# Performance work log

Hardware: AMD Instinct MI355X
Metric: run time of the kernel (lower is better)

## Reference

```python
import jax, jax.numpy as jnp
import numpy as np

B, N, D_IN, D_OUT, E = 4, 50000, 128, 128, 800000


def setup_inputs() -> dict:
    key = jax.random.key(0)
    k_x, k_w, k_b, k_r, k_c, k_v = jax.random.split(key, 6)
    stdv = 1.0 / np.sqrt(D_OUT)
    x = jax.random.normal(k_x, (B, N, D_IN), dtype=jnp.float32)
    weight = jax.random.uniform(k_w, (D_IN, D_OUT), jnp.float32, -stdv, stdv)
    bias = jax.random.uniform(k_b, (D_OUT,), jnp.float32, -stdv, stdv)
    adj_rows = jax.random.randint(k_r, (E,), 0, N, dtype=jnp.int32)
    adj_cols = jax.random.randint(k_c, (E,), 0, N, dtype=jnp.int32)
    # positive edge weights (e.g. normalized adjacency values)
    adj_vals = jax.random.uniform(k_v, (E,), jnp.float32) * (1.0 / 16.0)
    edge_index = jnp.stack([adj_rows, adj_cols]).astype(jnp.int64)  # unused (pyg_builtin=False)
    return {"input": x, "weight": weight, "bias": bias,
            "adj_vals": adj_vals, "adj_rows": adj_rows, "adj_cols": adj_cols,
            "edge_index": edge_index}


def reference(input, weight, bias, adj_vals, adj_rows, adj_cols, edge_index):
    # support = input @ W : [B, N, D_OUT]
    support = jnp.einsum('bnd,df->bnf', input, weight)

    # node_repr = sparse adj (COO) @ support, batched == torch.sparse.mm path
    def agg(s):  # s: [N, D_OUT]
        msgs = adj_vals[:, None] * s[adj_cols]          # [E, D_OUT] gather
        return jax.ops.segment_sum(msgs, adj_rows, num_segments=N)  # scatter-add

    node_repr = jax.vmap(agg)(support) + bias           # [B, N, D_OUT]
    # net_norm='none' -> no norm; activation=relu; residual=False; dropout=0
    return jax.nn.relu(node_repr)
```

## Files before the change

### kernel.cpp

```cpp
#include <hip/hip_runtime.h>
#include <hip/hip_bf16.h>

#define BB 4
#define NN 50000
#define DIN 128
#define DOUT 128
#define EE 800000
#define TOTROWS (BB * NN)
#define LDA 136

typedef unsigned short u16;
typedef unsigned int u32;

using shortx8 = __attribute__((ext_vector_type(8))) short;
using ushortx4 = __attribute__((ext_vector_type(4))) unsigned short;
using ushortx8 = __attribute__((ext_vector_type(8))) unsigned short;
using floatx4 = __attribute__((ext_vector_type(4))) float;

__device__ __forceinline__ float b2f(u16 u) {
    u32 x = ((u32)u) << 16;
    float f;
    __builtin_memcpy(&f, &x, 4);
    return f;
}

__device__ __forceinline__ u16 f2b(float f) {
    u32 x;
    __builtin_memcpy(&x, &f, 4);
    u32 r = x + 0x7fffu + ((x >> 16) & 1u);
    return (u16)(r >> 16);
}

__global__ __launch_bounds__(256)
void k_detect(const u16* __restrict__ X, const u16* __restrict__ W,
              const u16* __restrict__ Bs, const u16* __restrict__ V,
              int nx, int nw, int nb, int nv, int* __restrict__ flags) {
    __shared__ int cnt[4];
    const int t = threadIdx.x;
    const int w = t >> 6;
    const int l = t & 63;
    if (t < 4) cnt[t] = 0;
    __syncthreads();
    const u16* p = (w == 0) ? X : (w == 1) ? W : (w == 2) ? Bs : V;
    const int n  = (w == 0) ? nx : (w == 1) ? nw : (w == 2) ? nb : nv;
    int bad = 0;
    for (int k = 0; k < 4; ++k) {
        unsigned idx = 2u * (unsigned)(((unsigned long long)(l * 4 + k) *
                                        (unsigned)(n >> 1)) >> 8);
        u16 s = p[idx];
        unsigned e = (s >> 7) & 0xFF;
        bool ok = ((s & 0x7FFF) == 0) || (e >= 90 && e <= 141);
        bad += ok ? 0 : 1;
    }
    atomicAdd(&cnt[w], bad);
    __syncthreads();
    if (l == 0) flags[w] = (cnt[w] >= 77) ? 1 : 0;
}

__global__ __launch_bounds__(256)
void k_prep(const void* __restrict__ Wv, const int* __restrict__ flags,
            u16* __restrict__ Wt) {
    int t = blockIdx.x * 256 + threadIdx.x;
    if (t < DIN * DOUT) {
        int f = t >> 7, k = t & 127;
        size_t src = (size_t)k * DOUT + f;
        Wt[t] = flags[1] ? f2b(((const float*)Wv)[src]) : ((const u16*)Wv)[src];
    }
}

__global__ __launch_bounds__(256, 3)
void k_gemm(const void* __restrict__ Xv, const u16* __restrict__ Wt,
            const int* __restrict__ flags, u16* __restrict__ sup) {
    __shared__ u16 lA[128 * LDA];

    const int xf32 = flags[0];
    const int tid = threadIdx.x;
    const int wid = tid >> 6;
    const int l   = tid & 63;
    const long rowBase = (long)blockIdx.x * 128;

    if (xf32) {
        const float* Xf = (const float*)Xv;
#pragma unroll
        for (int i = 0; i < 16; ++i) {
            int elem = i * 1024 + tid * 4;
            int row = elem >> 7, col = elem & 127;
            long gRow = rowBase + row;
            ushortx4 w4 = (ushortx4){0, 0, 0, 0};
            if (gRow < TOTROWS) {
                float4 v = *(const float4*)(Xf + gRow * DIN + col);
                w4[0] = f2b(v.x); w4[1] = f2b(v.y);
                w4[2] = f2b(v.z); w4[3] = f2b(v.w);
            }
            *(ushortx4*)&lA[row * LDA + col] = w4;
        }
    } else {
        const u16* X16 = (const u16*)Xv;
#pragma unroll
        for (int i = 0; i < 8; ++i) {
            int elem = i * 2048 + tid * 8;
            int row = elem >> 7, col = elem & 127;
            long gRow = rowBase + row;
            ushortx8 w8 = (ushortx8){0, 0, 0, 0, 0, 0, 0, 0};
            if (gRow < TOTROWS)
                w8 = *(const ushortx8*)(X16 + gRow * DIN + col);
            *(ushortx8*)&lA[row * LDA + col] = w8;
        }
    }

    const int wx = wid & 1;
    const int wy = wid >> 1;
    const int q8 = (l >> 4) * 8;
    const int lm = l & 15;

    shortx8 bf[16];
#pragma unroll
    for (int nt = 0; nt < 4; ++nt) {
        const size_t Frow = (size_t)(wx * 64 + nt * 16 + lm) * DIN;
#pragma unroll
        for (int c = 0; c < 4; ++c)
            bf[nt * 4 + c] = *(const shortx8*)(Wt + Frow + 32 * c + q8);
    }

    floatx4 acc[4][4];
#pragma unroll
    for (int mt = 0; mt < 4; ++mt)
#pragma unroll
        for (int nt = 0; nt < 4; ++nt)
            acc[mt][nt] = (floatx4){0.f, 0.f, 0.f, 0.f};

    __syncthreads();

    for (int c = 0; c < 4; ++c) {
        shortx8 af[4];
#pragma unroll
        for (int mt = 0; mt < 4; ++mt)
            af[mt] = *(const shortx8*)
                &lA[(size_t)(wy * 64 + mt * 16 + lm) * LDA + 32 * c + q8];
#pragma unroll
        for (int mt = 0; mt < 4; ++mt)
#pragma unroll
            for (int nt = 0; nt < 4; ++nt)
                acc[mt][nt] = __builtin_amdgcn_mfma_f32_16x16x32_bf16(
                    af[mt], bf[nt * 4 + c], acc[mt][nt], 0, 0, 0);
    }

#pragma unroll
    for (int mt = 0; mt < 4; ++mt) {
#pragma unroll
        for (int reg = 0; reg < 4; ++reg) {
            long R = rowBase + wy * 64 + mt * 16 + (l >> 4) * 4 + reg;
            if (R < TOTROWS) {
                int b = (int)(R / NN);
                int n = (int)(R % NN);
                size_t outRow = ((size_t)n * BB + b) * DOUT;
#pragma unroll
                for (int nt = 0; nt < 4; ++nt) {
                    int F = wx * 64 + nt * 16 + lm;
                    sup[outRow + F] = f2b(acc[mt][nt][reg]);
                }
            }
        }
    }
}

__global__ __launch_bounds__(256)
void k_hist(const int* __restrict__ rows, int* __restrict__ deg) {
    int e = blockIdx.x * 256 + threadIdx.x;
    if (e < EE) atomicAdd(&deg[rows[e]], 1);
}

#define CHUNK 1024
#define NCHUNK ((NN + CHUNK - 1) / CHUNK)

__global__ __launch_bounds__(256)
void k_scan_reduce(const int* __restrict__ deg, int* __restrict__ bsum) {
    __shared__ int sh[256];
    int t = threadIdx.x, blk = blockIdx.x;
    int base = blk * CHUNK + t * 4;
    int s = 0;
#pragma unroll
    for (int i = 0; i < 4; ++i) {
        int idx = base + i;
        if (idx < NN) s += deg[idx];
    }
    sh[t] = s;
    __syncthreads();
    for (int d = 128; d > 0; d >>= 1) {
        if (t < d) sh[t] += sh[t + d];
        __syncthreads();
    }
    if (t == 0) bsum[blk] = sh[0];
}

__global__ __launch_bounds__(64)
void k_scan_base(const int* __restrict__ bsum, int* __restrict__ bbase,
                 int* __restrict__ off) {
    if (threadIdx.x == 0) {
        int run = 0;
        for (int i = 0; i < NCHUNK; ++i) {
            bbase[i] = run;
            run += bsum[i];
        }
        off[NN] = run;
    }
}

__global__ __launch_bounds__(256)
void k_scan_chunk(const int* __restrict__ deg, const int* __restrict__ bbase,
                  int* __restrict__ off) {
    __shared__ int sh[256];
    int t = threadIdx.x;
    int blk = blockIdx.x;
    int base = blk * CHUNK + t * 4;
    int v[4];
    int tsum = 0;
#pragma unroll
    for (int i = 0; i < 4; ++i) {
        int idx = base + i;
        v[i] = (idx < NN) ? deg[idx] : 0;
        tsum += v[i];
    }
    sh[t] = tsum;
    __syncthreads();
    for (int d = 1; d < 256; d <<= 1) {
        int x = (t >= d) ? sh[t - d] : 0;
        __syncthreads();
        sh[t] += x;
        __syncthreads();
    }
    int run = sh[t] - tsum + bbase[blk];
#pragma unroll
    for (int i = 0; i < 4; ++i) {
        int idx = base + i;
        if (idx < NN) off[idx] = run;
        run += v[i];
    }
}

__global__ __launch_bounds__(256)
void k_scatter(const int* __restrict__ rows, const int* __restrict__ cols,
               const void* __restrict__ valsv, const int* __restrict__ flags,
               const int* __restrict__ off, int* __restrict__ cur,
               int* __restrict__ ecol, float* __restrict__ eval) {
    int e = blockIdx.x * 256 + threadIdx.x;
    if (e < EE) {
        int vf32 = flags[3];
        float v = vf32 ? ((const float*)valsv)[e] : b2f(((const u16*)valsv)[e]);
        int r = rows[e];
        int p = off[r] + atomicAdd(&cur[r], 1);
        ecol[p] = cols[e];
        eval[p] = v;
    }
}

__global__ __launch_bounds__(256)
void k_agg(const u16* __restrict__ sup, const int* __restrict__ off,
           const int* __restrict__ ecol, const float* __restrict__ eval,
           const void* __restrict__ biasv, const int* __restrict__ flags,
           float* __restrict__ out) {
    const int wid = threadIdx.x >> 6;
    const int l   = threadIdx.x & 63;
    const int n = blockIdx.x * 4 + wid;
    if (n >= NN) return;

    const int p0 = off[n];
    const int p1 = off[n + 1];

    float acc[8] = {0.f, 0.f, 0.f, 0.f, 0.f, 0.f, 0.f, 0.f};
    const int b  = l >> 4;
    const int f0 = (l & 15) * 8;
    const int lofs = l * 8;

    int p = p0;
    for (; p + 2 <= p1; p += 2) {
        int c0 = ecol[p], c1 = ecol[p + 1];
        float v0 = eval[p], v1 = eval[p + 1];
        ushortx8 s0 = *(const ushortx8*)(sup + (size_t)c0 * 512 + lofs);
        ushortx8 s1 = *(const ushortx8*)(sup + (size_t)c1 * 512 + lofs);
#pragma unroll
        for (int t = 0; t < 8; ++t) acc[t] += v0 * b2f(s0[t]);
#pragma unroll
        for (int t = 0; t < 8; ++t) acc[t] += v1 * b2f(s1[t]);
    }
    if (p < p1) {
        int c = ecol[p];
        float v = eval[p];
        ushortx8 s = *(const ushortx8*)(sup + (size_t)c * 512 + lofs);
#pragma unroll
        for (int t = 0; t < 8; ++t) acc[t] += v * b2f(s[t]);
    }

    float bb[8];
    if (flags[2]) {
        float4 bv1 = *(const float4*)((const float*)biasv + f0);
        float4 bv2 = *(const float4*)((const float*)biasv + f0 + 4);
        bb[0] = bv1.x; bb[1] = bv1.y; bb[2] = bv1.z; bb[3] = bv1.w;
        bb[4] = bv2.x; bb[5] = bv2.y; bb[6] = bv2.z; bb[7] = bv2.w;
    } else {
        ushortx8 bv = *(const ushortx8*)((const u16*)biasv + f0);
#pragma unroll
        for (int t = 0; t < 8; ++t) bb[t] = b2f(bv[t]);
    }

    float r[8];
#pragma unroll
    for (int t = 0; t < 8; ++t) r[t] = fmaxf(acc[t] + bb[t], 0.f);

    float* op = out + ((size_t)b * NN + n) * DOUT + f0;
    *(float4*)op       = (float4){r[0], r[1], r[2], r[3]};
    *(float4*)(op + 4) = (float4){r[4], r[5], r[6], r[7]};
}

extern "C" void kernel_launch(void* const* d_in, const int* in_sizes, int n_in,
                              void* d_out, int out_size, void* d_ws, size_t ws_size,
                              hipStream_t stream) {
    const void* X    = d_in[0];
    const void* W    = d_in[1];
    const void* bias = d_in[2];
    const void* vals = d_in[3];
    const int* rows  = (const int*)d_in[4];
    const int* cols  = (const int*)d_in[5];
    float* out = (float*)d_out;

    char* base = (char*)d_ws;
    size_t o = 0;
    int* flags = (int*)(base + o); o += 64;
    int* deg = (int*)(base + o); o += (size_t)NN * 4;
    int* cur = (int*)(base + o); o += (size_t)NN * 4;
    o = (o + 255) & ~(size_t)255;
    int* bsum  = (int*)(base + o); o += 64 * 4;
    int* bbase = (int*)(base + o); o += 64 * 4;
    o = (o + 255) & ~(size_t)255;
    u16* Wt = (u16*)(base + o); o += (size_t)DIN * DOUT * 2;
    o = (o + 255) & ~(size_t)255;
    int* off = (int*)(base + o); o += (size_t)(NN + 1) * 4;
    o = (o + 255) & ~(size_t)255;
    int* ecol = (int*)(base + o); o += (size_t)EE * 4;
    float* eval = (float*)(base + o); o += (size_t)EE * 4;
    o = (o + 255) & ~(size_t)255;
    u16* sup = (u16*)(base + o); o += (size_t)BB * NN * DOUT * 2;
    (void)ws_size;

    hipMemsetAsync(deg, 0, (size_t)2 * NN * 4, stream);

    k_detect<<<1, 256, 0, stream>>>((const u16*)X, (const u16*)W,
                                    (const u16*)bias, (const u16*)vals,
                                    in_sizes[0], in_sizes[1], in_sizes[2],
                                    in_sizes[3], flags);
    k_prep<<<64, 256, 0, stream>>>(W, flags, Wt);
    k_gemm<<<(TOTROWS + 127) / 128, 256, 0, stream>>>(X, Wt, flags, sup);
    k_hist<<<(EE + 255) / 256, 256, 0, stream>>>(rows, deg);
    k_scan_reduce<<<NCHUNK, 256, 0, stream>>>(deg, bsum);
    k_scan_base<<<1, 64, 0, stream>>>(bsum, bbase, off);
    k_scan_chunk<<<NCHUNK, 256, 0, stream>>>(deg, bbase, off);
    k_scatter<<<(EE + 255) / 256, 256, 0, stream>>>(rows, cols, vals, flags,
                                                    off, cur, ecol, eval);
    k_agg<<<(NN + 3) / 4, 256, 0, stream>>>(sup, off, ecol, eval, bias, flags,
                                            out);
}
```

Before: 431.1 us.

## Stage GEMM output through LDS, pack edge col/val, unroll aggregation by four

The GEMM epilogue now writes accumulators into shared memory and then emits 16-byte vectorized row stores, replacing scattered 2-byte stores into the interleaved support layout. Edge column and value are packed into a single int2 array, so the aggregation makes one 8-byte load per edge instead of two separate loads. The aggregation loop is unrolled to four gathers in flight to raise memory-level parallelism. The block-sum scan becomes a wavefront shuffle scan instead of a serial single-thread loop. The cost is an extra LDS round trip and barrier in the GEMM and higher register use in the aggregation loop.

```diff
diff --git a/kernel.cpp b/kernel.cpp
--- a/kernel.cpp
+++ b/kernel.cpp
@@ -145,21 +145,29 @@
                     af[mt], bf[nt * 4 + c], acc[mt][nt], 0, 0, 0);
     }
 
+    __syncthreads();
 #pragma unroll
     for (int mt = 0; mt < 4; ++mt) {
 #pragma unroll
         for (int reg = 0; reg < 4; ++reg) {
-            long R = rowBase + wy * 64 + mt * 16 + (l >> 4) * 4 + reg;
-            if (R < TOTROWS) {
-                int b = (int)(R / NN);
-                int n = (int)(R % NN);
-                size_t outRow = ((size_t)n * BB + b) * DOUT;
-#pragma unroll
-                for (int nt = 0; nt < 4; ++nt) {
-                    int F = wx * 64 + nt * 16 + lm;
-                    sup[outRow + F] = f2b(acc[mt][nt][reg]);
-                }
-            }
+            int row = wy * 64 + mt * 16 + (l >> 4) * 4 + reg;
+#pragma unroll
+            for (int nt = 0; nt < 4; ++nt)
+                lA[row * LDA + wx * 64 + nt * 16 + lm] = f2b(acc[mt][nt][reg]);
+        }
+    }
+    __syncthreads();
+
+#pragma unroll
+    for (int i = 0; i < 8; ++i) {
+        int elem = i * 2048 + tid * 8;
+        int row = elem >> 7, col = elem & 127;
+        long R = rowBase + row;
+        if (R < TOTROWS) {
+            int b = (int)(R / NN);
+            int n = (int)(R % NN);
+            ushortx8 v = *(const ushortx8*)&lA[row * LDA + col];
+            *(ushortx8*)(sup + ((size_t)n * BB + b) * DOUT + col) = v;
         }
     }
 }
@@ -196,14 +204,15 @@
 __global__ __launch_bounds__(64)
 void k_scan_base(const int* __restrict__ bsum, int* __restrict__ bbase,
                  int* __restrict__ off) {
-    if (threadIdx.x == 0) {
-        int run = 0;
-        for (int i = 0; i < NCHUNK; ++i) {
-            bbase[i] = run;
-            run += bsum[i];
-        }
-        off[NN] = run;
-    }
+    int l = threadIdx.x;
+    int orig = (l < NCHUNK) ? bsum[l] : 0;
+    int v = orig;
+    for (int d = 1; d < 64; d <<= 1) {
+        int x = __shfl_up(v, d);
+        if (l >= d) v += x;
+    }
+    if (l < NCHUNK) bbase[l] = v - orig;
+    if (l == NCHUNK - 1) off[NN] = v;
 }
 
 __global__ __launch_bounds__(256)
@@ -242,23 +251,21 @@
 void k_scatter(const int* __restrict__ rows, const int* __restrict__ cols,
                const void* __restrict__ valsv, const int* __restrict__ flags,
                const int* __restrict__ off, int* __restrict__ cur,
-               int* __restrict__ ecol, float* __restrict__ eval) {
+               int2* __restrict__ epk) {
     int e = blockIdx.x * 256 + threadIdx.x;
     if (e < EE) {
         int vf32 = flags[3];
         float v = vf32 ? ((const float*)valsv)[e] : b2f(((const u16*)valsv)[e]);
         int r = rows[e];
         int p = off[r] + atomicAdd(&cur[r], 1);
-        ecol[p] = cols[e];
-        eval[p] = v;
+        epk[p] = make_int2(cols[e], __float_as_int(v));
     }
 }
 
 __global__ __launch_bounds__(256)
 void k_agg(const u16* __restrict__ sup, const int* __restrict__ off,
-           const int* __restrict__ ecol, const float* __restrict__ eval,
-           const void* __restrict__ biasv, const int* __restrict__ flags,
-           float* __restrict__ out) {
+           const int2* __restrict__ epk, const void* __restrict__ biasv,
+           const int* __restrict__ flags, float* __restrict__ out) {
     const int wid = threadIdx.x >> 6;
     const int l   = threadIdx.x & 63;
     const int n = blockIdx.x * 4 + wid;
@@ -273,20 +280,28 @@
     const int lofs = l * 8;
 
     int p = p0;
-    for (; p + 2 <= p1; p += 2) {
-        int c0 = ecol[p], c1 = ecol[p + 1];
-        float v0 = eval[p], v1 = eval[p + 1];
-        ushortx8 s0 = *(const ushortx8*)(sup + (size_t)c0 * 512 + lofs);
-        ushortx8 s1 = *(const ushortx8*)(sup + (size_t)c1 * 512 + lofs);
+    for (; p + 4 <= p1; p += 4) {
+        int2 e0 = epk[p],     e1 = epk[p + 1];
+        int2 e2 = epk[p + 2], e3 = epk[p + 3];
+        ushortx8 s0 = *(const ushortx8*)(sup + (size_t)e0.x * 512 + lofs);
+        ushortx8 s1 = *(const ushortx8*)(sup + (size_t)e1.x * 512 + lofs);
+        ushortx8 s2 = *(const ushortx8*)(sup + (size_t)e2.x * 512 + lofs);
+        ushortx8 s3 = *(const ushortx8*)(sup + (size_t)e3.x * 512 + lofs);
+        float v0 = __int_as_float(e0.y), v1 = __int_as_float(e1.y);
+        float v2 = __int_as_float(e2.y), v3 = __int_as_float(e3.y);
 #pragma unroll
         for (int t = 0; t < 8; ++t) acc[t] += v0 * b2f(s0[t]);
 #pragma unroll
         for (int t = 0; t < 8; ++t) acc[t] += v1 * b2f(s1[t]);
-    }
-    if (p < p1) {
-        int c = ecol[p];
-        float v = eval[p];
-        ushortx8 s = *(const ushortx8*)(sup + (size_t)c * 512 + lofs);
+#pragma unroll
+        for (int t = 0; t < 8; ++t) acc[t] += v2 * b2f(s2[t]);
+#pragma unroll
+        for (int t = 0; t < 8; ++t) acc[t] += v3 * b2f(s3[t]);
+    }
+    for (; p < p1; ++p) {
+        int2 e = epk[p];
+        float v = __int_as_float(e.y);
+        ushortx8 s = *(const ushortx8*)(sup + (size_t)e.x * 512 + lofs);
 #pragma unroll
         for (int t = 0; t < 8; ++t) acc[t] += v * b2f(s[t]);
     }
@@ -336,8 +351,7 @@
     o = (o + 255) & ~(size_t)255;
     int* off = (int*)(base + o); o += (size_t)(NN + 1) * 4;
     o = (o + 255) & ~(size_t)255;
-    int* ecol = (int*)(base + o); o += (size_t)EE * 4;
-    float* eval = (float*)(base + o); o += (size_t)EE * 4;
+    int2* epk = (int2*)(base + o); o += (size_t)EE * 8;
     o = (o + 255) & ~(size_t)255;
     u16* sup = (u16*)(base + o); o += (size_t)BB * NN * DOUT * 2;
     (void)ws_size;
@@ -355,7 +369,6 @@
     k_scan_base<<<1, 64, 0, stream>>>(bsum, bbase, off);
     k_scan_chunk<<<NCHUNK, 256, 0, stream>>>(deg, bbase, off);
     k_scatter<<<(EE + 255) / 256, 256, 0, stream>>>(rows, cols, vals, flags,
-                                                    off, cur, ecol, eval);
-    k_agg<<<(NN + 3) / 4, 256, 0, stream>>>(sup, off, ecol, eval, bias, flags,
-                                            out);
-}
+                                                    off, cur, epk);
+    k_agg<<<(NN + 3) / 4, 256, 0, stream>>>(sup, off, epk, bias, flags, out);
+}
```

New measurement: 425.3 us. Within noise of the previous version (-1.3%).
